# Kernel tuning notes

Hardware: AMD Instinct MI355X
Metric: run time of the kernel (lower is better)

Reference implementation:

```python
import jax, jax.numpy as jnp
import numpy as np

N, E, H, G, L = 50000, 640000, 128, 8, 3

def setup_inputs() -> dict:
    key = jax.random.key(0)
    ks = jax.random.split(key, 10)
    s = 1.0 / np.sqrt(H)
    return {
        "x": jax.random.normal(ks[0], (N, H), jnp.float32),
        "query": jax.random.normal(ks[1], (G, H), jnp.float32),
        "Wl": jax.random.normal(ks[2], (L, H, H), jnp.float32) * s,
        "bl": jax.random.normal(ks[3], (L, H), jnp.float32) * s,
        "Wr": jax.random.normal(ks[4], (L, H, H), jnp.float32) * s,
        "Wlin": jax.random.normal(ks[5], (H, H), jnp.float32) * s,
        "blin": jax.random.normal(ks[6], (H,), jnp.float32) * s,
        "edge_index": jax.random.randint(ks[7], (2, E), 0, N, jnp.int64),
        "batch_vec": jnp.sort(jax.random.randint(ks[8], (N,), 0, G, jnp.int64)),
    }

def reference(x, query, Wl, bl, Wr, Wlin, blin, edge_index, batch_vec):
    src, dst = edge_index[0], edge_index[1]
    n = x.shape[0]
    for i in range(L):
        # SAGEConv(aggr='max'): gather neighbor feats, scatter-max to dst
        m = jax.ops.segment_max(x[src], dst, num_segments=n)  # [N,H]
        m = jnp.where(jnp.isfinite(m), m, 0.0)  # isolated nodes -> 0 (PyG)
        x = jax.nn.relu(m @ Wl[i].T + bl[i] + x @ Wr[i].T)
    x = x @ Wlin.T + blin  # encoder final linear
    # cosine scoring per graph, vectorized via batch_vec
    xn = x / jnp.linalg.norm(x, axis=1, keepdims=True).clip(1e-12)
    qn = query / jnp.linalg.norm(query, axis=1, keepdims=True).clip(1e-12)
    scores = jnp.sum(xn * qn[batch_vec], axis=1)  # [N]
    return scores
```

## Files before the change

### kernel.cpp

```cpp
#include <hip/hip_runtime.h>
#include <math.h>

#define H 128

typedef _Float16 half8 __attribute__((ext_vector_type(8)));
typedef float f32x16 __attribute__((ext_vector_type(16)));
typedef int int4v __attribute__((ext_vector_type(4)));

__device__ __forceinline__ half8 h8max(half8 a, half8 b) {
#if defined(__has_builtin) && __has_builtin(__builtin_elementwise_max)
    return __builtin_elementwise_max(a, b);
#else
    half8 r;
#pragma unroll
    for (int j = 0; j < 8; ++j) r[j] = a[j] > b[j] ? a[j] : b[j];
    return r;
#endif
}

__device__ __forceinline__ half8 h8shfl_xor(half8 v, int mask) {
    int4v iv;
    __builtin_memcpy(&iv, &v, 16);
#pragma unroll
    for (int j = 0; j < 4; ++j) iv[j] = __shfl_xor(iv[j], mask, 64);
    half8 r;
    __builtin_memcpy(&r, &iv, 16);
    return r;
}


__global__ __launch_bounds__(256) void scan_atomic(const int* __restrict__ deg,
                                                   int* __restrict__ offsets,
                                                   int* __restrict__ gcur, int N) {
    __shared__ int buf[256];
    __shared__ int sbase;
    int tid = threadIdx.x;
    int i = blockIdx.x * 256 + tid;
    int v = (i < N) ? deg[i] : 0;
    int incl = v;
    buf[tid] = v;
    __syncthreads();
#pragma unroll
    for (int off = 1; off < 256; off <<= 1) {
        int t = (tid >= off) ? buf[tid - off] : 0;
        __syncthreads();
        incl += t;
        buf[tid] = incl;
        __syncthreads();
    }
    if (tid == 255) sbase = atomicAdd(gcur, incl);
    __syncthreads();
    if (i < N) offsets[i] = sbase + incl - v;
}

__global__ __launch_bounds__(256) void fill_adj(const int* __restrict__ ei, int E,
                                                const int* __restrict__ offsets,
                                                int* __restrict__ cursor,
                                                int* __restrict__ adj) {
    int e = blockIdx.x * 256 + threadIdx.x;
    if (e < E) {
        int s = ei[e];
        int d = ei[E + e];
        int pos = atomicAdd(&cursor[d], 1);
        adj[offsets[d] + pos] = s;
    }
}


__global__ __launch_bounds__(256) void prep_all(
    const int* __restrict__ ei, int E, int* __restrict__ deg,
    const float* __restrict__ x, const float* __restrict__ query,
    const float* __restrict__ Wl, const float* __restrict__ Wr,
    const float* __restrict__ Wlin, _Float16* __restrict__ xh,
    _Float16* __restrict__ wimg, float* __restrict__ qn, int n8, int HB, int SB,
    int WB) {
    int b = blockIdx.x;
    int tid = threadIdx.x;
    if (b < HB) {
        int e = b * 256 + tid;
        if (e < E) atomicAdd(&deg[ei[E + e]], 1);
    } else if (b < HB + SB) {
        int i = (b - HB) * 256 + tid;
        if (i < n8) {
            const float4* x4 = (const float4*)x;
            float4 u = x4[(size_t)i * 2], v = x4[(size_t)i * 2 + 1];
            float f[8] = {u.x, u.y, u.z, u.w, v.x, v.y, v.z, v.w};
            half8 h;
#pragma unroll
            for (int j = 0; j < 8; ++j) h[j] = (_Float16)f[j];
            *(half8*)(xh + (size_t)i * 8) = h;
        }
    } else if (b < HB + SB + WB) {
        int gidx = (b - HB - SB) * 256 + tid;
        if (gidx < 7 * 2048) {
            int mat = gidx / 2048;
            int rem = gidx - mat * 2048;
            if (mat == 6) {
                int n = rem >> 4;
                int g = rem & 15;
                const float* p = Wlin + n * H + g * 8;
                half8 h, l;
#pragma unroll
                for (int j = 0; j < 8; ++j) {
                    float v = p[j];
                    _Float16 hh = (_Float16)v;
                    h[j] = hh;
                    l[j] = (_Float16)(v - (float)hh);
                }
                int kc4 = g >> 2, gpc = g & 3;
                int posB = (gpc + (n & 3) + ((n >> 2) & 3)) & 3;
                size_t base =
                    (size_t)mat * 32768 + (size_t)kc4 * 8192 + n * 32 + posB * 8;
                *(half8*)(wimg + base) = h;
                *(half8*)(wimg + base + 4096) = l;
            } else {
                int kc4 = rem >> 9;
                int r2 = rem & 511;
                int s = r2 >> 6;
                int lane = r2 & 63;
                int ks = s >> 2;
                int colgrp = s & 3;
                int lhi = lane >> 5, l31 = lane & 31;
                int n = colgrp * 32 + l31;
                int g16 = kc4 * 4 + ks * 2 + lhi;
                const float* src = (mat & 1) ? Wr + (mat >> 1) * H * H
                                             : Wl + (mat >> 1) * H * H;
                const float* p = src + n * H + g16 * 8;
                half8 h, l;
#pragma unroll
                for (int j = 0; j < 8; ++j) {
                    float v = p[j];
                    _Float16 hh = (_Float16)v;
                    h[j] = hh;
                    l[j] = (_Float16)(v - (float)hh);
                }
                size_t base = (size_t)mat * 32768 + (size_t)kc4 * 8192 +
                              (size_t)s * 1024 + (size_t)lane * 16;
                *(half8*)(wimg + base) = h;
                *(half8*)(wimg + base + 8) = l;
            }
        }
    } else {
        int g = b - HB - SB - WB;
        __shared__ float part[4];
        float v = (tid < 128) ? query[g * H + tid] : 0.f;
        float ss = v * v;
#pragma unroll
        for (int off = 32; off > 0; off >>= 1) ss += __shfl_xor(ss, off, 64);
        if ((tid & 63) == 0) part[tid >> 6] = ss;
        __syncthreads();
        float tot = part[0] + part[1];
        if (tid < 128) qn[g * H + tid] = v / fmaxf(sqrtf(tot), 1e-12f);
    }
}


__global__ __launch_bounds__(256, 6) void layer_fused(
    const half8* __restrict__ Xh, const int* __restrict__ deg,
    const int* __restrict__ offsets, const int* __restrict__ adj,
    const _Float16* __restrict__ Bimg, const float* __restrict__ bias,
    _Float16* __restrict__ Yh, int N) {
    __shared__ __align__(16) _Float16 sU[4096];
    __shared__ __align__(16) _Float16 sX[4096];

    int tid = threadIdx.x;
    int w = tid >> 6;
    int lane = tid & 63;
    int l31 = lane & 31;
    int lhi = lane >> 5;
    int n0 = blockIdx.x * 32;

    {
        int sub = lane >> 4;
        int lf = lane & 15;
        const _Float16 ni = (_Float16)(-INFINITY);
        const half8 ninf = {ni, ni, ni, ni, ni, ni, ni, ni};
        const half8 hz = {(_Float16)0.f, (_Float16)0.f, (_Float16)0.f, (_Float16)0.f,
                          (_Float16)0.f, (_Float16)0.f, (_Float16)0.f, (_Float16)0.f};
        int nd = n0 + w * 8 + (lf & 7);
        int ndc = nd < N ? nd : N - 1;
        int e0v = offsets[ndc];
        int degv = (nd < N) ? deg[ndc] : 0;

        int dmx = degv;
#pragma unroll
        for (int off = 1; off <= 8; off <<= 1) {
            int t = __shfl_xor(dmx, off, 64);
            dmx = t > dmx ? t : dmx;
        }

        if (dmx <= 32) {
            int adjf[4];
#pragma unroll
            for (int rr = 0; rr < 4; ++rr) {
                int i = 2 * rr + (lane >> 5);
                int e0 = __shfl(e0v, i, 64);
                int d = __shfl(degv, i, 64);
                int s = lane & 31;
                int p = d > 0 ? e0 + (s < d ? s : d - 1) : 0;
                adjf[rr] = adj[p];
            }
#pragma unroll
            for (int i = 0; i < 8; ++i) {
                int d = __shfl(degv, i, 64);
                int dm1 = d > 0 ? d - 1 : 0;
                int srcb = (i & 1) << 5;
                int j0 = sub, j1 = 4 + sub, j2 = 8 + sub, j3 = 12 + sub;
                int i0 = __shfl(adjf[i >> 1], srcb | (j0 < d ? j0 : dm1), 64);
                int i1 = __shfl(adjf[i >> 1], srcb | (j1 < d ? j1 : dm1), 64);
                int i2 = __shfl(adjf[i >> 1], srcb | (j2 < d ? j2 : dm1), 64);
                int i3 = __shfl(adjf[i >> 1], srcb | (j3 < d ? j3 : dm1), 64);
                half8 v0 = Xh[(size_t)i0 * 16 + lf];
                half8 v1 = Xh[(size_t)i1 * 16 + lf];
                half8 v2 = Xh[(size_t)i2 * 16 + lf];
                half8 v3 = Xh[(size_t)i3 * 16 + lf];
                half8 acc = h8max(h8max(v0, v1), h8max(v2, v3));
                if (d > 16) {
                    int j4 = 16 + sub, j5 = 20 + sub, j6 = 24 + sub, j7 = 28 + sub;
                    int i4 = __shfl(adjf[i >> 1], srcb | (j4 < d ? j4 : dm1), 64);
                    int i5 = __shfl(adjf[i >> 1], srcb | (j5 < d ? j5 : dm1), 64);
                    int i6 = __shfl(adjf[i >> 1], srcb | (j6 < d ? j6 : dm1), 64);
                    int i7 = __shfl(adjf[i >> 1], srcb | (j7 < d ? j7 : dm1), 64);
                    half8 u0 = Xh[(size_t)i4 * 16 + lf];
                    half8 u1 = Xh[(size_t)i5 * 16 + lf];
                    half8 u2 = Xh[(size_t)i6 * 16 + lf];
                    half8 u3 = Xh[(size_t)i7 * 16 + lf];
                    acc = h8max(acc, h8max(h8max(u0, u1), h8max(u2, u3)));
                }
                acc = h8max(acc, h8shfl_xor(acc, 16));
                acc = h8max(acc, h8shfl_xor(acc, 32));
                if (d == 0) acc = hz;
                int row = w * 8 + i;
                if (sub == 0) *(half8*)&sU[row * 128 + ((lf ^ (row & 15)) << 3)] = acc;
            }
        } else {
            for (int i = 0; i < 8; ++i) {
                int e0 = __shfl(e0v, i, 64);
                int d = __shfl(degv, i, 64);
                int row = w * 8 + i;
                half8 acc = ninf;
                for (int base = 0; base < d; base += 16) {
                    half8 v[4];
#pragma unroll
                    for (int q = 0; q < 4; ++q) {
                        int j = base + q * 4 + sub;
                        int idx = adj[e0 + (j < d ? j : d - 1)];
                        v[q] = Xh[(size_t)idx * 16 + lf];
                    }
                    acc = h8max(acc, h8max(h8max(v[0], v[1]), h8max(v[2], v[3])));
                }
                acc = h8max(acc, h8shfl_xor(acc, 16));
                acc = h8max(acc, h8shfl_xor(acc, 32));
                if (d == 0) acc = hz;
                if (sub == 0) *(half8*)&sU[row * 128 + ((lf ^ (row & 15)) << 3)] = acc;
            }
        }
    }
    __syncthreads();

    {
        const half8 hz = {(_Float16)0.f, (_Float16)0.f, (_Float16)0.f, (_Float16)0.f,
                          (_Float16)0.f, (_Float16)0.f, (_Float16)0.f, (_Float16)0.f};
#pragma unroll
        for (int t = 0; t < 2; ++t) {
            int idx = tid + t * 256;
            int row = idx >> 4;
            int g = idx & 15;
            int nn = n0 + row;
            half8 h = hz;
            if (nn < N) h = Xh[(size_t)nn * 16 + g];
            *(half8*)&sX[row * 128 + ((g ^ (row & 15)) << 3)] = h;
        }
    }

    f32x16 acc;
    {
        float bvv = bias[w * 32 + l31];
#pragma unroll
        for (int r = 0; r < 16; ++r) acc[r] = bvv;
    }

    int rl = l31;

#pragma unroll
    for (int kc4 = 0; kc4 < 4; ++kc4) {
#pragma unroll
        for (int ks = 0; ks < 2; ++ks) {
            int g16 = kc4 * 4 + ks * 2 + lhi;
            int posA = g16 ^ (rl & 15);
            half8 ah = *(const half8*)&sU[rl * 128 + posA * 8];
            size_t boff =
                (size_t)kc4 * 8192 + (size_t)(ks * 4 + w) * 1024 + (size_t)lane * 16;
            half8 bh = *(const half8*)&Bimg[boff];
            half8 bl2 = *(const half8*)&Bimg[boff + 8];
            acc = __builtin_amdgcn_mfma_f32_32x32x16_f16(ah, bh, acc, 0, 0, 0);
            acc = __builtin_amdgcn_mfma_f32_32x32x16_f16(ah, bl2, acc, 0, 0, 0);
        }
    }

    __syncthreads();

    const _Float16* Br = Bimg + 32768;
#pragma unroll
    for (int kc4 = 0; kc4 < 4; ++kc4) {
#pragma unroll
        for (int ks = 0; ks < 2; ++ks) {
            int g16 = kc4 * 4 + ks * 2 + lhi;
            int posA = g16 ^ (rl & 15);
            half8 ah = *(const half8*)&sX[rl * 128 + posA * 8];
            size_t boff =
                (size_t)kc4 * 8192 + (size_t)(ks * 4 + w) * 1024 + (size_t)lane * 16;
            half8 bh = *(const half8*)&Br[boff];
            half8 bl2 = *(const half8*)&Br[boff + 8];
            acc = __builtin_amdgcn_mfma_f32_32x32x16_f16(ah, bh, acc, 0, 0, 0);
            acc = __builtin_amdgcn_mfma_f32_32x32x16_f16(ah, bl2, acc, 0, 0, 0);
        }
    }

    int n = w * 32 + l31;
#pragma unroll
    for (int r = 0; r < 16; ++r) {
        int row = n0 + (r & 3) + 8 * (r >> 2) + 4 * lhi;
        if (row < N) Yh[(size_t)row * H + n] = (_Float16)fmaxf(acc[r], 0.f);
    }
}


__global__ __launch_bounds__(256) void final_mfma6(
    const half8* __restrict__ Xh, const _Float16* __restrict__ Bimg,
    const float* __restrict__ blin, const float* __restrict__ qn,
    const int* __restrict__ bv, float* __restrict__ out, int N) {
    __shared__ __align__(16) _Float16 sA[9216];
    __shared__ __align__(16) _Float16 sB[8192];

    int tid = threadIdx.x;
    int w = tid >> 6;
    int lane = tid & 63;
    int l31 = lane & 31;
    int lhi = lane >> 5;
    int n0 = blockIdx.x * 128;

    int arow = n0 + w * 32 + l31;
    arow = arow < N ? arow : N - 1;
    int gl = bv[arow];

    f32x16 acc[4];
#pragma unroll
    for (int nt = 0; nt < 4; ++nt) {
        float b = blin[nt * 32 + l31];
#pragma unroll
        for (int r = 0; r < 16; ++r) acc[nt][r] = b;
    }

    int rl = w * 32 + l31;

    for (int kc4 = 0; kc4 < 4; ++kc4) {
        if (kc4) __syncthreads();
        {
            const half8* bsrc = (const half8*)(Bimg + (size_t)kc4 * 8192);
            half8* bdst = (half8*)sB;
#pragma unroll
            for (int i = 0; i < 4; ++i) bdst[tid + i * 256] = bsrc[tid + i * 256];
        }
        if ((kc4 & 1) == 0) {
            int kc64 = kc4 >> 1;
#pragma unroll
            for (int i = 0; i < 4; ++i) {
                int idx = tid + i * 256;
                int row = idx >> 3;
                int gp8 = idx & 7;
                int nn = n0 + row;
                half8 h = {(_Float16)0.f, (_Float16)0.f, (_Float16)0.f, (_Float16)0.f,
                           (_Float16)0.f, (_Float16)0.f, (_Float16)0.f, (_Float16)0.f};
                if (nn < N) h = Xh[(size_t)nn * 16 + kc64 * 8 + gp8];
                int pos8 = (gp8 + (row & 7) + ((row >> 3) & 7)) & 7;
                *(half8*)&sA[row * 72 + pos8 * 8] = h;
            }
        }
        __syncthreads();
#pragma unroll
        for (int ks = 0; ks < 2; ++ks) {
            int gp8 = (kc4 & 1) * 4 + ks * 2 + lhi;
            int posA8 = (gp8 + (rl & 7) + ((rl >> 3) & 7)) & 7;
            half8 ah = *(const half8*)&sA[rl * 72 + posA8 * 8];
#pragma unroll
            for (int nt = 0; nt < 4; ++nt) {
                int nn = nt * 32 + l31;
                int gpc = ks * 2 + lhi;
                int posB = (gpc + (nn & 3) + ((nn >> 2) & 3)) & 3;
                half8 bh = *(const half8*)&sB[nn * 32 + posB * 8];
                half8 bl2 = *(const half8*)&sB[4096 + nn * 32 + posB * 8];
                acc[nt] = __builtin_amdgcn_mfma_f32_32x32x16_f16(ah, bh, acc[nt], 0, 0, 0);
                acc[nt] = __builtin_amdgcn_mfma_f32_32x32x16_f16(ah, bl2, acc[nt], 0, 0, 0);
            }
        }
    }

#pragma unroll
    for (int r = 0; r < 16; ++r) {
        int rloc = (r & 3) + 8 * (r >> 2) + 4 * lhi;
        int row = n0 + w * 32 + rloc;
        int g = __shfl(gl, rloc, 32);
        float ss = 0.f, sd = 0.f;
#pragma unroll
        for (int nt = 0; nt < 4; ++nt) {
            float y = acc[nt][r];
            float q = qn[(size_t)g * H + nt * 32 + l31];
            ss = fmaf(y, y, ss);
            sd = fmaf(y, q, sd);
        }
#pragma unroll
        for (int off = 1; off <= 16; off <<= 1) {
            ss += __shfl_xor(ss, off, 64);
            sd += __shfl_xor(sd, off, 64);
        }
        if (l31 == 0 && row < N) out[row] = sd / fmaxf(sqrtf(ss), 1e-12f);
    }
}


extern "C" void kernel_launch(void* const* d_in, const int* in_sizes, int n_in,
                              void* d_out, int out_size, void* d_ws, size_t ws_size,
                              hipStream_t stream) {
    const float* x = (const float*)d_in[0];
    const float* query = (const float*)d_in[1];
    const float* Wl = (const float*)d_in[2];
    const float* bl = (const float*)d_in[3];
    const float* Wr = (const float*)d_in[4];
    const float* Wlin = (const float*)d_in[5];
    const float* blin = (const float*)d_in[6];
    const int* ei = (const int*)d_in[7];
    const int* bv = (const int*)d_in[8];
    float* out = (float*)d_out;

    const int N = in_sizes[0] / H;
    const int E = in_sizes[7] / 2;
    const int G = in_sizes[1] / H;

    char* p = (char*)d_ws;
    auto alloc = [&](size_t bytes) {
        char* r = p;
        p += (bytes + 255) & ~(size_t)255;
        return r;
    };
    int* deg = (int*)alloc((size_t)(2 * N + 1) * sizeof(int));
    int* cursor = deg + N;
    int* gcur = deg + 2 * N;
    int* offsets = (int*)alloc((size_t)N * sizeof(int));
    int* adj = (int*)alloc((size_t)E * sizeof(int));
    float* qn = (float*)alloc((size_t)G * H * sizeof(float));
    _Float16* wimg = (_Float16*)alloc((size_t)7 * 32768 * sizeof(_Float16));
    size_t actH = (size_t)N * H * sizeof(_Float16);
    _Float16* xah = (_Float16*)alloc(actH);
    _Float16* xbh = (_Float16*)alloc(actH);

    hipMemsetAsync(deg, 0, (size_t)(2 * N + 1) * sizeof(int), stream);

    const int n8 = N * H / 8;
    const int HB = (E + 255) / 256;
    const int SB = (n8 + 255) / 256;
    const int WB = (7 * 2048 + 255) / 256;
    prep_all<<<HB + SB + WB + G, 256, 0, stream>>>(ei, E, deg, x, query, Wl, Wr,
                                                   Wlin, xah, wimg, qn, n8, HB,
                                                   SB, WB);
    scan_atomic<<<(N + 255) / 256, 256, 0, stream>>>(deg, offsets, gcur, N);
    fill_adj<<<(E + 255) / 256, 256, 0, stream>>>(ei, E, offsets, cursor, adj);

    const int NGm = (N + 31) / 32;
    const int NGf = (N + 127) / 128;

    layer_fused<<<NGm, 256, 0, stream>>>(
        (const half8*)xah, deg, offsets, adj, wimg + (size_t)0 * 65536,
        bl + 0 * H, xbh, N);
    layer_fused<<<NGm, 256, 0, stream>>>(
        (const half8*)xbh, deg, offsets, adj, wimg + (size_t)1 * 65536,
        bl + 1 * H, xah, N);
    layer_fused<<<NGm, 256, 0, stream>>>(
        (const half8*)xah, deg, offsets, adj, wimg + (size_t)2 * 65536,
        bl + 2 * H, xbh, N);
    final_mfma6<<<NGf, 256, 0, stream>>>(
        (const half8*)xbh, wimg + (size_t)6 * 32768, blin, qn, bv, out, N);
}
```

Before: 269.9 us.

## Precompute padded fixed-width neighbor table and hoist self-feature and weight loads

Adds a build_adjp kernel that, once per call, writes a fixed 32-slot padded neighbor-index table per node (split into two 16-wide arrays), clamping to the last neighbor or the node itself. The layer kernel then reads neighbor indices with coalesced loads and no offset lookup, replacing the per-layer clamp arithmetic and the dependent offsets-to-adj load chain. It also moves the self-feature staging into shared memory and the first weight fragment load ahead of the gather, and drops one block barrier. The cost is an extra kernel launch plus about 6.4MB of index table that must be written and then read in each layer.

Result: no change. 273.3 us (+1.2%).

```diff
diff --git a/kernel.cpp b/kernel.cpp
--- a/kernel.cpp
+++ b/kernel.cpp
@@ -63,6 +63,24 @@
         int d = ei[E + e];
         int pos = atomicAdd(&cursor[d], 1);
         adj[offsets[d] + pos] = s;
+    }
+}
+
+__global__ __launch_bounds__(256) void build_adjp(
+    const int* __restrict__ deg, const int* __restrict__ offsets,
+    const int* __restrict__ adj, int* __restrict__ adjp,
+    int* __restrict__ adjp2, int N) {
+    int idx = blockIdx.x * 256 + threadIdx.x;
+    int total = N * 16;
+    if (idx < total) {
+        int n = idx >> 4, s = idx & 15;
+        int d = deg[n];
+        adjp[idx] = d > 0 ? adj[offsets[n] + (s < d ? s : d - 1)] : n;
+    } else if (idx < 2 * total) {
+        int i2 = idx - total;
+        int n = i2 >> 4, s = (i2 & 15) + 16;
+        int d = deg[n];
+        adjp2[i2] = d > 0 ? adj[offsets[n] + (s < d ? s : d - 1)] : n;
     }
 }
 
@@ -158,6 +176,7 @@
 __global__ __launch_bounds__(256, 6) void layer_fused(
     const half8* __restrict__ Xh, const int* __restrict__ deg,
     const int* __restrict__ offsets, const int* __restrict__ adj,
+    const int* __restrict__ adjp, const int* __restrict__ adjp2,
     const _Float16* __restrict__ Bimg, const float* __restrict__ bias,
     _Float16* __restrict__ Yh, int N) {
     __shared__ __align__(16) _Float16 sU[4096];
@@ -170,57 +189,74 @@
     int lhi = lane >> 5;
     int n0 = blockIdx.x * 32;
 
+    const half8 hz = {(_Float16)0.f, (_Float16)0.f, (_Float16)0.f, (_Float16)0.f,
+                      (_Float16)0.f, (_Float16)0.f, (_Float16)0.f, (_Float16)0.f};
+
+    {
+#pragma unroll
+        for (int t = 0; t < 2; ++t) {
+            int idx = tid + t * 256;
+            int row = idx >> 4;
+            int g = idx & 15;
+            int nn = n0 + row;
+            half8 h = hz;
+            if (nn < N) h = Xh[(size_t)nn * 16 + g];
+            *(half8*)&sX[row * 128 + ((g ^ (row & 15)) << 3)] = h;
+        }
+    }
+
+    half8 pbh, pbl;
+    {
+        size_t b00 = (size_t)w * 1024 + (size_t)lane * 16;
+        pbh = *(const half8*)&Bimg[b00];
+        pbl = *(const half8*)&Bimg[b00 + 8];
+    }
+
     {
         int sub = lane >> 4;
         int lf = lane & 15;
         const _Float16 ni = (_Float16)(-INFINITY);
         const half8 ninf = {ni, ni, ni, ni, ni, ni, ni, ni};
-        const half8 hz = {(_Float16)0.f, (_Float16)0.f, (_Float16)0.f, (_Float16)0.f,
-                          (_Float16)0.f, (_Float16)0.f, (_Float16)0.f, (_Float16)0.f};
-        int nd = n0 + w * 8 + (lf & 7);
-        int ndc = nd < N ? nd : N - 1;
-        int e0v = offsets[ndc];
-        int degv = (nd < N) ? deg[ndc] : 0;
+        int nd8 = n0 + w * 8;
+        int nn = nd8 + (lane & 7);
+        int degv = (nn < N) ? deg[nn] : 0;
 
         int dmx = degv;
 #pragma unroll
-        for (int off = 1; off <= 8; off <<= 1) {
+        for (int off = 1; off <= 4; off <<= 1) {
             int t = __shfl_xor(dmx, off, 64);
             dmx = t > dmx ? t : dmx;
         }
 
         if (dmx <= 32) {
-            int adjf[4];
-#pragma unroll
-            for (int rr = 0; rr < 4; ++rr) {
-                int i = 2 * rr + (lane >> 5);
-                int e0 = __shfl(e0v, i, 64);
-                int d = __shfl(degv, i, 64);
-                int s = lane & 31;
-                int p = d > 0 ? e0 + (s < d ? s : d - 1) : 0;
-                adjf[rr] = adj[p];
-            }
+            int c0 = nd8 + (lane >> 4);
+            c0 = c0 < N ? c0 : N - 1;
+            int c1 = nd8 + 4 + (lane >> 4);
+            c1 = c1 < N ? c1 : N - 1;
+            int b0 = c0 * 16 + (lane & 15);
+            int b1 = c1 * 16 + (lane & 15);
+            int r0 = adjp[b0];
+            int r1 = adjp[b1];
+            int r2 = adjp2[b0];
+            int r3 = adjp2[b1];
 #pragma unroll
             for (int i = 0; i < 8; ++i) {
                 int d = __shfl(degv, i, 64);
-                int dm1 = d > 0 ? d - 1 : 0;
-                int srcb = (i & 1) << 5;
-                int j0 = sub, j1 = 4 + sub, j2 = 8 + sub, j3 = 12 + sub;
-                int i0 = __shfl(adjf[i >> 1], srcb | (j0 < d ? j0 : dm1), 64);
-                int i1 = __shfl(adjf[i >> 1], srcb | (j1 < d ? j1 : dm1), 64);
-                int i2 = __shfl(adjf[i >> 1], srcb | (j2 < d ? j2 : dm1), 64);
-                int i3 = __shfl(adjf[i >> 1], srcb | (j3 < d ? j3 : dm1), 64);
+                int sel = ((i & 3) << 4) | sub;
+                int i0 = __shfl(i < 4 ? r0 : r1, sel, 64);
+                int i1 = __shfl(i < 4 ? r0 : r1, sel | 4, 64);
+                int i2 = __shfl(i < 4 ? r0 : r1, sel | 8, 64);
+                int i3 = __shfl(i < 4 ? r0 : r1, sel | 12, 64);
                 half8 v0 = Xh[(size_t)i0 * 16 + lf];
                 half8 v1 = Xh[(size_t)i1 * 16 + lf];
                 half8 v2 = Xh[(size_t)i2 * 16 + lf];
                 half8 v3 = Xh[(size_t)i3 * 16 + lf];
                 half8 acc = h8max(h8max(v0, v1), h8max(v2, v3));
                 if (d > 16) {
-                    int j4 = 16 + sub, j5 = 20 + sub, j6 = 24 + sub, j7 = 28 + sub;
-                    int i4 = __shfl(adjf[i >> 1], srcb | (j4 < d ? j4 : dm1), 64);
-                    int i5 = __shfl(adjf[i >> 1], srcb | (j5 < d ? j5 : dm1), 64);
-                    int i6 = __shfl(adjf[i >> 1], srcb | (j6 < d ? j6 : dm1), 64);
-                    int i7 = __shfl(adjf[i >> 1], srcb | (j7 < d ? j7 : dm1), 64);
+                    int i4 = __shfl(i < 4 ? r2 : r3, sel, 64);
+                    int i5 = __shfl(i < 4 ? r2 : r3, sel | 4, 64);
+                    int i6 = __shfl(i < 4 ? r2 : r3, sel | 8, 64);
+                    int i7 = __shfl(i < 4 ? r2 : r3, sel | 12, 64);
                     half8 u0 = Xh[(size_t)i4 * 16 + lf];
                     half8 u1 = Xh[(size_t)i5 * 16 + lf];
                     half8 u2 = Xh[(size_t)i6 * 16 + lf];
@@ -234,6 +270,8 @@
                 if (sub == 0) *(half8*)&sU[row * 128 + ((lf ^ (row & 15)) << 3)] = acc;
             }
         } else {
+            int ndc = nn < N ? nn : N - 1;
+            int e0v = offsets[ndc];
             for (int i = 0; i < 8; ++i) {
                 int e0 = __shfl(e0v, i, 64);
                 int d = __shfl(degv, i, 64);
@@ -258,21 +296,6 @@
     }
     __syncthreads();
 
-    {
-        const half8 hz = {(_Float16)0.f, (_Float16)0.f, (_Float16)0.f, (_Float16)0.f,
-                          (_Float16)0.f, (_Float16)0.f, (_Float16)0.f, (_Float16)0.f};
-#pragma unroll
-        for (int t = 0; t < 2; ++t) {
-            int idx = tid + t * 256;
-            int row = idx >> 4;
-            int g = idx & 15;
-            int nn = n0 + row;
-            half8 h = hz;
-            if (nn < N) h = Xh[(size_t)nn * 16 + g];
-            *(half8*)&sX[row * 128 + ((g ^ (row & 15)) << 3)] = h;
-        }
-    }
-
     f32x16 acc;
     {
         float bvv = bias[w * 32 + l31];
@@ -289,16 +312,20 @@
             int g16 = kc4 * 4 + ks * 2 + lhi;
             int posA = g16 ^ (rl & 15);
             half8 ah = *(const half8*)&sU[rl * 128 + posA * 8];
-            size_t boff =
-                (size_t)kc4 * 8192 + (size_t)(ks * 4 + w) * 1024 + (size_t)lane * 16;
-            half8 bh = *(const half8*)&Bimg[boff];
-            half8 bl2 = *(const half8*)&Bimg[boff + 8];
+            half8 bh, bl2;
+            if (kc4 == 0 && ks == 0) {
+                bh = pbh;
+                bl2 = pbl;
+            } else {
+                size_t boff = (size_t)kc4 * 8192 + (size_t)(ks * 4 + w) * 1024 +
+                              (size_t)lane * 16;
+                bh = *(const half8*)&Bimg[boff];
+                bl2 = *(const half8*)&Bimg[boff + 8];
+            }
             acc = __builtin_amdgcn_mfma_f32_32x32x16_f16(ah, bh, acc, 0, 0, 0);
             acc = __builtin_amdgcn_mfma_f32_32x32x16_f16(ah, bl2, acc, 0, 0, 0);
         }
     }
-
-    __syncthreads();
 
     const _Float16* Br = Bimg + 32768;
 #pragma unroll
@@ -448,6 +475,8 @@
     int* gcur = deg + 2 * N;
     int* offsets = (int*)alloc((size_t)N * sizeof(int));
     int* adj = (int*)alloc((size_t)E * sizeof(int));
+    int* adjp = (int*)alloc((size_t)N * 16 * sizeof(int));
+    int* adjp2 = (int*)alloc((size_t)N * 16 * sizeof(int));
     float* qn = (float*)alloc((size_t)G * H * sizeof(float));
     _Float16* wimg = (_Float16*)alloc((size_t)7 * 32768 * sizeof(_Float16));
     size_t actH = (size_t)N * H * sizeof(_Float16);
@@ -465,19 +494,21 @@
                                                    SB, WB);
     scan_atomic<<<(N + 255) / 256, 256, 0, stream>>>(deg, offsets, gcur, N);
     fill_adj<<<(E + 255) / 256, 256, 0, stream>>>(ei, E, offsets, cursor, adj);
+    build_adjp<<<(2 * N * 16 + 255) / 256, 256, 0, stream>>>(deg, offsets, adj,
+                                                             adjp, adjp2, N);
 
     const int NGm = (N + 31) / 32;
     const int NGf = (N + 127) / 128;
 
     layer_fused<<<NGm, 256, 0, stream>>>(
-        (const half8*)xah, deg, offsets, adj, wimg + (size_t)0 * 65536,
-        bl + 0 * H, xbh, N);
+        (const half8*)xah, deg, offsets, adj, adjp, adjp2,
+        wimg + (size_t)0 * 65536, bl + 0 * H, xbh, N);
     layer_fused<<<NGm, 256, 0, stream>>>(
-        (const half8*)xbh, deg, offsets, adj, wimg + (size_t)1 * 65536,
-        bl + 1 * H, xah, N);
+        (const half8*)xbh, deg, offsets, adj, adjp, adjp2,
+        wimg + (size_t)1 * 65536, bl + 1 * H, xah, N);
     layer_fused<<<NGm, 256, 0, stream>>>(
-        (const half8*)xah, deg, offsets, adj, wimg + (size_t)2 * 65536,
-        bl + 2 * H, xbh, N);
+        (const half8*)xah, deg, offsets, adj, adjp, adjp2,
+        wimg + (size_t)2 * 65536, bl + 2 * H, xbh, N);
     final_mfma6<<<NGf, 256, 0, stream>>>(
         (const half8*)xbh, wimg + (size_t)6 * 32768, blin, qn, bv, out, N);
 }
```

## Fuse final linear and cosine scoring into last layer; add padded 32-slot adjacency

Applied to the files above, without the earlier changes.

Folds the final encoder linear and per-graph cosine scoring into the third layer kernel, so that layer's fp16 activations no longer go to global memory and come back, and one launch is dropped. Adds a zero-initialised fixed-stride 32-entry adjacency array filled alongside CSR, so low-degree nodes fetch neighbours without reading offsets. It also moves the self-feature tile load ahead of aggregation and removes a barrier. The costs are an extra N*32 int memset and scattered writes in fill_adj, and a heavier final layer kernel.

New measurement: 283.3 us. 1.05x slower.

```diff
diff --git a/kernel.cpp b/kernel.cpp
--- a/kernel.cpp
+++ b/kernel.cpp
@@ -56,13 +56,15 @@
 __global__ __launch_bounds__(256) void fill_adj(const int* __restrict__ ei, int E,
                                                 const int* __restrict__ offsets,
                                                 int* __restrict__ cursor,
-                                                int* __restrict__ adj) {
+                                                int* __restrict__ adj,
+                                                int* __restrict__ adjp32) {
     int e = blockIdx.x * 256 + threadIdx.x;
     if (e < E) {
         int s = ei[e];
         int d = ei[E + e];
         int pos = atomicAdd(&cursor[d], 1);
         adj[offsets[d] + pos] = s;
+        if (pos < 32) adjp32[(size_t)d * 32 + pos] = s;
     }
 }
 
@@ -95,50 +97,31 @@
         if (gidx < 7 * 2048) {
             int mat = gidx / 2048;
             int rem = gidx - mat * 2048;
-            if (mat == 6) {
-                int n = rem >> 4;
-                int g = rem & 15;
-                const float* p = Wlin + n * H + g * 8;
-                half8 h, l;
-#pragma unroll
-                for (int j = 0; j < 8; ++j) {
-                    float v = p[j];
-                    _Float16 hh = (_Float16)v;
-                    h[j] = hh;
-                    l[j] = (_Float16)(v - (float)hh);
-                }
-                int kc4 = g >> 2, gpc = g & 3;
-                int posB = (gpc + (n & 3) + ((n >> 2) & 3)) & 3;
-                size_t base =
-                    (size_t)mat * 32768 + (size_t)kc4 * 8192 + n * 32 + posB * 8;
-                *(half8*)(wimg + base) = h;
-                *(half8*)(wimg + base + 4096) = l;
-            } else {
-                int kc4 = rem >> 9;
-                int r2 = rem & 511;
-                int s = r2 >> 6;
-                int lane = r2 & 63;
-                int ks = s >> 2;
-                int colgrp = s & 3;
-                int lhi = lane >> 5, l31 = lane & 31;
-                int n = colgrp * 32 + l31;
-                int g16 = kc4 * 4 + ks * 2 + lhi;
-                const float* src = (mat & 1) ? Wr + (mat >> 1) * H * H
-                                             : Wl + (mat >> 1) * H * H;
-                const float* p = src + n * H + g16 * 8;
-                half8 h, l;
-#pragma unroll
-                for (int j = 0; j < 8; ++j) {
-                    float v = p[j];
-                    _Float16 hh = (_Float16)v;
-                    h[j] = hh;
-                    l[j] = (_Float16)(v - (float)hh);
-                }
-                size_t base = (size_t)mat * 32768 + (size_t)kc4 * 8192 +
-                              (size_t)s * 1024 + (size_t)lane * 16;
-                *(half8*)(wimg + base) = h;
-                *(half8*)(wimg + base + 8) = l;
-            }
+            int kc4 = rem >> 9;
+            int r2 = rem & 511;
+            int s = r2 >> 6;
+            int lane = r2 & 63;
+            int ks = s >> 2;
+            int colgrp = s & 3;
+            int lhi = lane >> 5, l31 = lane & 31;
+            int n = colgrp * 32 + l31;
+            int g16 = kc4 * 4 + ks * 2 + lhi;
+            const float* src = (mat == 6) ? Wlin
+                             : ((mat & 1) ? Wr + (mat >> 1) * H * H
+                                          : Wl + (mat >> 1) * H * H);
+            const float* p = src + n * H + g16 * 8;
+            half8 h, l;
+#pragma unroll
+            for (int j = 0; j < 8; ++j) {
+                float v = p[j];
+                _Float16 hh = (_Float16)v;
+                h[j] = hh;
+                l[j] = (_Float16)(v - (float)hh);
+            }
+            size_t base = (size_t)mat * 32768 + (size_t)kc4 * 8192 +
+                          (size_t)s * 1024 + (size_t)lane * 16;
+            *(half8*)(wimg + base) = h;
+            *(half8*)(wimg + base + 8) = l;
         }
     } else {
         int g = b - HB - SB - WB;
@@ -155,11 +138,15 @@
 }
 
 
+template <bool FINAL>
 __global__ __launch_bounds__(256, 6) void layer_fused(
     const half8* __restrict__ Xh, const int* __restrict__ deg,
     const int* __restrict__ offsets, const int* __restrict__ adj,
-    const _Float16* __restrict__ Bimg, const float* __restrict__ bias,
-    _Float16* __restrict__ Yh, int N) {
+    const int* __restrict__ adjp32, const _Float16* __restrict__ Bimg,
+    const float* __restrict__ bias, _Float16* __restrict__ Yh,
+    const _Float16* __restrict__ BimgF, const float* __restrict__ blin,
+    const float* __restrict__ qn, const int* __restrict__ bv,
+    float* __restrict__ out, int N) {
     __shared__ __align__(16) _Float16 sU[4096];
     __shared__ __align__(16) _Float16 sX[4096];
 
@@ -170,57 +157,70 @@
     int lhi = lane >> 5;
     int n0 = blockIdx.x * 32;
 
+    const half8 hz = {(_Float16)0.f, (_Float16)0.f, (_Float16)0.f, (_Float16)0.f,
+                      (_Float16)0.f, (_Float16)0.f, (_Float16)0.f, (_Float16)0.f};
+
+    {
+#pragma unroll
+        for (int t = 0; t < 2; ++t) {
+            int idx = tid + t * 256;
+            int row = idx >> 4;
+            int g = idx & 15;
+            int nn = n0 + row;
+            half8 h = hz;
+            if (nn < N) h = Xh[(size_t)nn * 16 + g];
+            *(half8*)&sX[row * 128 + ((g ^ (row & 15)) << 3)] = h;
+        }
+    }
+
     {
         int sub = lane >> 4;
         int lf = lane & 15;
         const _Float16 ni = (_Float16)(-INFINITY);
         const half8 ninf = {ni, ni, ni, ni, ni, ni, ni, ni};
-        const half8 hz = {(_Float16)0.f, (_Float16)0.f, (_Float16)0.f, (_Float16)0.f,
-                          (_Float16)0.f, (_Float16)0.f, (_Float16)0.f, (_Float16)0.f};
-        int nd = n0 + w * 8 + (lf & 7);
-        int ndc = nd < N ? nd : N - 1;
-        int e0v = offsets[ndc];
-        int degv = (nd < N) ? deg[ndc] : 0;
+        int nd8 = n0 + w * 8;
+        int nn = nd8 + (lane & 7);
+        int degv = (nn < N) ? deg[nn] : 0;
 
         int dmx = degv;
 #pragma unroll
-        for (int off = 1; off <= 8; off <<= 1) {
+        for (int off = 1; off <= 4; off <<= 1) {
             int t = __shfl_xor(dmx, off, 64);
             dmx = t > dmx ? t : dmx;
         }
 
         if (dmx <= 32) {
-            int adjf[4];
-#pragma unroll
-            for (int rr = 0; rr < 4; ++rr) {
-                int i = 2 * rr + (lane >> 5);
-                int e0 = __shfl(e0v, i, 64);
-                int d = __shfl(degv, i, 64);
-                int s = lane & 31;
-                int p = d > 0 ? e0 + (s < d ? s : d - 1) : 0;
-                adjf[rr] = adj[p];
-            }
+            int c0 = nd8 + (lane >> 4);
+            c0 = c0 < N ? c0 : N - 1;
+            int c1 = nd8 + 4 + (lane >> 4);
+            c1 = c1 < N ? c1 : N - 1;
+            int r0 = adjp32[(size_t)c0 * 32 + (lane & 15)];
+            int r1 = adjp32[(size_t)c1 * 32 + (lane & 15)];
+            int r2 = adjp32[(size_t)c0 * 32 + 16 + (lane & 15)];
+            int r3 = adjp32[(size_t)c1 * 32 + 16 + (lane & 15)];
 #pragma unroll
             for (int i = 0; i < 8; ++i) {
                 int d = __shfl(degv, i, 64);
-                int dm1 = d > 0 ? d - 1 : 0;
-                int srcb = (i & 1) << 5;
+                int base = (i & 3) << 4;
                 int j0 = sub, j1 = 4 + sub, j2 = 8 + sub, j3 = 12 + sub;
-                int i0 = __shfl(adjf[i >> 1], srcb | (j0 < d ? j0 : dm1), 64);
-                int i1 = __shfl(adjf[i >> 1], srcb | (j1 < d ? j1 : dm1), 64);
-                int i2 = __shfl(adjf[i >> 1], srcb | (j2 < d ? j2 : dm1), 64);
-                int i3 = __shfl(adjf[i >> 1], srcb | (j3 < d ? j3 : dm1), 64);
+                int i0 = __shfl(i < 4 ? r0 : r1, base | (j0 < d ? j0 : 0), 64);
+                int i1 = __shfl(i < 4 ? r0 : r1, base | (j1 < d ? j1 : 0), 64);
+                int i2 = __shfl(i < 4 ? r0 : r1, base | (j2 < d ? j2 : 0), 64);
+                int i3 = __shfl(i < 4 ? r0 : r1, base | (j3 < d ? j3 : 0), 64);
                 half8 v0 = Xh[(size_t)i0 * 16 + lf];
                 half8 v1 = Xh[(size_t)i1 * 16 + lf];
                 half8 v2 = Xh[(size_t)i2 * 16 + lf];
                 half8 v3 = Xh[(size_t)i3 * 16 + lf];
                 half8 acc = h8max(h8max(v0, v1), h8max(v2, v3));
                 if (d > 16) {
-                    int j4 = 16 + sub, j5 = 20 + sub, j6 = 24 + sub, j7 = 28 + sub;
-                    int i4 = __shfl(adjf[i >> 1], srcb | (j4 < d ? j4 : dm1), 64);
-                    int i5 = __shfl(adjf[i >> 1], srcb | (j5 < d ? j5 : dm1), 64);
-                    int i6 = __shfl(adjf[i >> 1], srcb | (j6 < d ? j6 : dm1), 64);
-                    int i7 = __shfl(adjf[i >> 1], srcb | (j7 < d ? j7 : dm1), 64);
+                    int k4 = (16 + sub) < d ? sub : 0;
+                    int k5 = (20 + sub) < d ? 4 + sub : 0;
+                    int k6 = (24 + sub) < d ? 8 + sub : 0;
+                    int k7 = (28 + sub) < d ? 12 + sub : 0;
+                    int i4 = __shfl(i < 4 ? r2 : r3, base | k4, 64);
+                    int i5 = __shfl(i < 4 ? r2 : r3, base | k5, 64);
+                    int i6 = __shfl(i < 4 ? r2 : r3, base | k6, 64);
+                    int i7 = __shfl(i < 4 ? r2 : r3, base | k7, 64);
                     half8 u0 = Xh[(size_t)i4 * 16 + lf];
                     half8 u1 = Xh[(size_t)i5 * 16 + lf];
                     half8 u2 = Xh[(size_t)i6 * 16 + lf];
@@ -234,6 +234,8 @@
                 if (sub == 0) *(half8*)&sU[row * 128 + ((lf ^ (row & 15)) << 3)] = acc;
             }
         } else {
+            int ndc = nn < N ? nn : N - 1;
+            int e0v = offsets[ndc];
             for (int i = 0; i < 8; ++i) {
                 int e0 = __shfl(e0v, i, 64);
                 int d = __shfl(degv, i, 64);
@@ -258,21 +260,6 @@
     }
     __syncthreads();
 
-    {
-        const half8 hz = {(_Float16)0.f, (_Float16)0.f, (_Float16)0.f, (_Float16)0.f,
-                          (_Float16)0.f, (_Float16)0.f, (_Float16)0.f, (_Float16)0.f};
-#pragma unroll
-        for (int t = 0; t < 2; ++t) {
-            int idx = tid + t * 256;
-            int row = idx >> 4;
-            int g = idx & 15;
-            int nn = n0 + row;
-            half8 h = hz;
-            if (nn < N) h = Xh[(size_t)nn * 16 + g];
-            *(half8*)&sX[row * 128 + ((g ^ (row & 15)) << 3)] = h;
-        }
-    }
-
     f32x16 acc;
     {
         float bvv = bias[w * 32 + l31];
@@ -281,6 +268,7 @@
     }
 
     int rl = l31;
+    int col = w * 32 + l31;
 
 #pragma unroll
     for (int kc4 = 0; kc4 < 4; ++kc4) {
@@ -298,8 +286,6 @@
         }
     }
 
-    __syncthreads();
-
     const _Float16* Br = Bimg + 32768;
 #pragma unroll
     for (int kc4 = 0; kc4 < 4; ++kc4) {
@@ -317,104 +303,79 @@
         }
     }
 
-    int n = w * 32 + l31;
-#pragma unroll
-    for (int r = 0; r < 16; ++r) {
-        int row = n0 + (r & 3) + 8 * (r >> 2) + 4 * lhi;
-        if (row < N) Yh[(size_t)row * H + n] = (_Float16)fmaxf(acc[r], 0.f);
-    }
-}
-
-
-__global__ __launch_bounds__(256) void final_mfma6(
-    const half8* __restrict__ Xh, const _Float16* __restrict__ Bimg,
-    const float* __restrict__ blin, const float* __restrict__ qn,
-    const int* __restrict__ bv, float* __restrict__ out, int N) {
-    __shared__ __align__(16) _Float16 sA[9216];
-    __shared__ __align__(16) _Float16 sB[8192];
-
-    int tid = threadIdx.x;
-    int w = tid >> 6;
-    int lane = tid & 63;
-    int l31 = lane & 31;
-    int lhi = lane >> 5;
-    int n0 = blockIdx.x * 128;
-
-    int arow = n0 + w * 32 + l31;
-    arow = arow < N ? arow : N - 1;
-    int gl = bv[arow];
-
-    f32x16 acc[4];
-#pragma unroll
-    for (int nt = 0; nt < 4; ++nt) {
-        float b = blin[nt * 32 + l31];
-#pragma unroll
-        for (int r = 0; r < 16; ++r) acc[nt][r] = b;
-    }
-
-    int rl = w * 32 + l31;
-
-    for (int kc4 = 0; kc4 < 4; ++kc4) {
-        if (kc4) __syncthreads();
+    if constexpr (!FINAL) {
+#pragma unroll
+        for (int r = 0; r < 16; ++r) {
+            int row = n0 + (r & 3) + 8 * (r >> 2) + 4 * lhi;
+            if (row < N) Yh[(size_t)row * H + col] = (_Float16)fmaxf(acc[r], 0.f);
+        }
+    } else {
+        __syncthreads();
+#pragma unroll
+        for (int r = 0; r < 16; ++r) {
+            int rloc = (r & 3) + 8 * (r >> 2) + 4 * lhi;
+            sU[rloc * 128 + (((col >> 3) ^ (rloc & 15)) << 3) + (col & 7)] =
+                (_Float16)fmaxf(acc[r], 0.f);
+        }
+        f32x16 acc2;
         {
-            const half8* bsrc = (const half8*)(Bimg + (size_t)kc4 * 8192);
-            half8* bdst = (half8*)sB;
-#pragma unroll
-            for (int i = 0; i < 4; ++i) bdst[tid + i * 256] = bsrc[tid + i * 256];
-        }
-        if ((kc4 & 1) == 0) {
-            int kc64 = kc4 >> 1;
-#pragma unroll
-            for (int i = 0; i < 4; ++i) {
-                int idx = tid + i * 256;
-                int row = idx >> 3;
-                int gp8 = idx & 7;
-                int nn = n0 + row;
-                half8 h = {(_Float16)0.f, (_Float16)0.f, (_Float16)0.f, (_Float16)0.f,
-                           (_Float16)0.f, (_Float16)0.f, (_Float16)0.f, (_Float16)0.f};
-                if (nn < N) h = Xh[(size_t)nn * 16 + kc64 * 8 + gp8];
-                int pos8 = (gp8 + (row & 7) + ((row >> 3) & 7)) & 7;
-                *(half8*)&sA[row * 72 + pos8 * 8] = h;
-            }
-        }
-        __syncthreads();
-#pragma unroll
-        for (int ks = 0; ks < 2; ++ks) {
-            int gp8 = (kc4 & 1) * 4 + ks * 2 + lhi;
-            int posA8 = (gp8 + (rl & 7) + ((rl >> 3) & 7)) & 7;
-            half8 ah = *(const half8*)&sA[rl * 72 + posA8 * 8];
-#pragma unroll
-            for (int nt = 0; nt < 4; ++nt) {
-                int nn = nt * 32 + l31;
-                int gpc = ks * 2 + lhi;
-                int posB = (gpc + (nn & 3) + ((nn >> 2) & 3)) & 3;
-                half8 bh = *(const half8*)&sB[nn * 32 + posB * 8];
-                half8 bl2 = *(const half8*)&sB[4096 + nn * 32 + posB * 8];
-                acc[nt] = __builtin_amdgcn_mfma_f32_32x32x16_f16(ah, bh, acc[nt], 0, 0, 0);
-                acc[nt] = __builtin_amdgcn_mfma_f32_32x32x16_f16(ah, bl2, acc[nt], 0, 0, 0);
-            }
-        }
-    }
-
-#pragma unroll
-    for (int r = 0; r < 16; ++r) {
-        int rloc = (r & 3) + 8 * (r >> 2) + 4 * lhi;
-        int row = n0 + w * 32 + rloc;
-        int g = __shfl(gl, rloc, 32);
-        float ss = 0.f, sd = 0.f;
-#pragma unroll
-        for (int nt = 0; nt < 4; ++nt) {
-            float y = acc[nt][r];
-            float q = qn[(size_t)g * H + nt * 32 + l31];
-            ss = fmaf(y, y, ss);
-            sd = fmaf(y, q, sd);
-        }
-#pragma unroll
-        for (int off = 1; off <= 16; off <<= 1) {
-            ss += __shfl_xor(ss, off, 64);
-            sd += __shfl_xor(sd, off, 64);
-        }
-        if (l31 == 0 && row < N) out[row] = sd / fmaxf(sqrtf(ss), 1e-12f);
+            float b = blin[col];
+#pragma unroll
+            for (int r = 0; r < 16; ++r) acc2[r] = b;
+        }
+        int arow = n0 + l31;
+        arow = arow < N ? arow : N - 1;
+        int gl = bv[arow];
+        __syncthreads();
+
+#pragma unroll
+        for (int kc4 = 0; kc4 < 4; ++kc4) {
+#pragma unroll
+            for (int ks = 0; ks < 2; ++ks) {
+                int g16 = kc4 * 4 + ks * 2 + lhi;
+                int posA = g16 ^ (rl & 15);
+                half8 ah = *(const half8*)&sU[rl * 128 + posA * 8];
+                size_t boff = (size_t)kc4 * 8192 + (size_t)(ks * 4 + w) * 1024 +
+                              (size_t)lane * 16;
+                half8 bh = *(const half8*)&BimgF[boff];
+                half8 bl2 = *(const half8*)&BimgF[boff + 8];
+                acc2 = __builtin_amdgcn_mfma_f32_32x32x16_f16(ah, bh, acc2, 0, 0, 0);
+                acc2 = __builtin_amdgcn_mfma_f32_32x32x16_f16(ah, bl2, acc2, 0, 0, 0);
+            }
+        }
+
+        float* sP = (float*)sX;
+#pragma unroll
+        for (int r = 0; r < 16; ++r) {
+            int rloc = (r & 3) + 8 * (r >> 2) + 4 * lhi;
+            int g = __shfl(gl, rloc, 32);
+            float y = acc2[r];
+            float q = qn[(size_t)g * H + col];
+            float ss = y * y;
+            float sd = y * q;
+#pragma unroll
+            for (int off = 1; off <= 16; off <<= 1) {
+                ss += __shfl_xor(ss, off, 64);
+                sd += __shfl_xor(sd, off, 64);
+            }
+            if (l31 == 0) {
+                sP[(rloc * 4 + w) * 2] = ss;
+                sP[(rloc * 4 + w) * 2 + 1] = sd;
+            }
+        }
+        __syncthreads();
+        if (tid < 32) {
+            int row = n0 + tid;
+            if (row < N) {
+                float ss = 0.f, sd = 0.f;
+#pragma unroll
+                for (int q = 0; q < 4; ++q) {
+                    ss += sP[(tid * 4 + q) * 2];
+                    sd += sP[(tid * 4 + q) * 2 + 1];
+                }
+                out[row] = sd / fmaxf(sqrtf(ss), 1e-12f);
+            }
+        }
     }
 }
 
@@ -448,6 +409,7 @@
     int* gcur = deg + 2 * N;
     int* offsets = (int*)alloc((size_t)N * sizeof(int));
     int* adj = (int*)alloc((size_t)E * sizeof(int));
+    int* adjp32 = (int*)alloc((size_t)N * 32 * sizeof(int));
     float* qn = (float*)alloc((size_t)G * H * sizeof(float));
     _Float16* wimg = (_Float16*)alloc((size_t)7 * 32768 * sizeof(_Float16));
     size_t actH = (size_t)N * H * sizeof(_Float16);
@@ -455,6 +417,7 @@
     _Float16* xbh = (_Float16*)alloc(actH);
 
     hipMemsetAsync(deg, 0, (size_t)(2 * N + 1) * sizeof(int), stream);
+    hipMemsetAsync(adjp32, 0, (size_t)N * 32 * sizeof(int), stream);
 
     const int n8 = N * H / 8;
     const int HB = (E + 255) / 256;
@@ -464,20 +427,18 @@
                                                    Wlin, xah, wimg, qn, n8, HB,
                                                    SB, WB);
     scan_atomic<<<(N + 255) / 256, 256, 0, stream>>>(deg, offsets, gcur, N);
-    fill_adj<<<(E + 255) / 256, 256, 0, stream>>>(ei, E, offsets, cursor, adj);
+    fill_adj<<<(E + 255) / 256, 256, 0, stream>>>(ei, E, offsets, cursor, adj,
+                                                  adjp32);
 
     const int NGm = (N + 31) / 32;
-    const int NGf = (N + 127) / 128;
-
-    layer_fused<<<NGm, 256, 0, stream>>>(
-        (const half8*)xah, deg, offsets, adj, wimg + (size_t)0 * 65536,
-        bl + 0 * H, xbh, N);
-    layer_fused<<<NGm, 256, 0, stream>>>(
-        (const half8*)xbh, deg, offsets, adj, wimg + (size_t)1 * 65536,
-        bl + 1 * H, xah, N);
-    layer_fused<<<NGm, 256, 0, stream>>>(
-        (const half8*)xah, deg, offsets, adj, wimg + (size_t)2 * 65536,
-        bl + 2 * H, xbh, N);
-    final_mfma6<<<NGf, 256, 0, stream>>>(
-        (const half8*)xbh, wimg + (size_t)6 * 32768, blin, qn, bv, out, N);
-}
+
+    layer_fused<false><<<NGm, 256, 0, stream>>>(
+        (const half8*)xah, deg, offsets, adj, adjp32, wimg + (size_t)0 * 65536,
+        bl + 0 * H, xbh, nullptr, nullptr, nullptr, nullptr, nullptr, N);
+    layer_fused<false><<<NGm, 256, 0, stream>>>(
+        (const half8*)xbh, deg, offsets, adj, adjp32, wimg + (size_t)1 * 65536,
+        bl + 1 * H, xah, nullptr, nullptr, nullptr, nullptr, nullptr, N);
+    layer_fused<true><<<NGm, 256, 0, stream>>>(
+        (const half8*)xah, deg, offsets, adj, adjp32, wimg + (size_t)2 * 65536,
+        bl + 2 * H, nullptr, wimg + (size_t)6 * 32768, blin, qn, bv, out, N);
+}
```
